# Optimization experiments

Hardware: AMD Instinct MI355X
Metric: run time of the kernel (lower is better)

The kernel has to match this reference:

```python
import jax, jax.numpy as jnp
import numpy as np

T, B, N = 1024, 1024, 64
BETA = 0.9          # bank LIF leak
THRESH = 1.0        # bank threshold
BETA_RO = 0.9       # readout leak
THRESH_RO = 1.0     # readout threshold
CHOSEN_W1 = 0.7
UTE = 1.01


def setup_inputs() -> dict:
    key = jax.random.key(0)
    # sparse binary spike input [T,B,2]
    spike_seq = (jax.random.uniform(key, (T, B, 2)) < 0.05).astype(jnp.float32)
    delays = jnp.arange(1, N + 1, dtype=jnp.int32)
    # per-neuron weights: w1 = chosen_w1, w2 = ute - beta**delay * w1
    w1 = jnp.full((N,), CHOSEN_W1, dtype=jnp.float32)
    w2 = (UTE - (BETA ** delays.astype(jnp.float32)) * CHOSEN_W1).astype(jnp.float32)
    W = jnp.stack([w1, w2], axis=1)  # [N,2]
    return {"spike_seq": spike_seq, "W": W, "delays": delays}


def reference(spike_seq, W, delays):
    Tn, Bn, _ = spike_seq.shape
    Nn = W.shape[0]
    BIG = jnp.iinfo(jnp.int32).max

    def step(carry, xt):
        x_t, t = xt
        bank_mem, ro_mem, inhibit, inhibit_time, winner = carry
        # ---- bank of N LIF neurons (snntorch Leaky, reset='subtract') ----
        cur = x_t @ W.T                                      # [B,N]
        reset = jnp.where(bank_mem > THRESH, THRESH, 0.0)    # reset from prev mem
        bank_mem = BETA * bank_mem + cur - reset
        spk = jnp.where(bank_mem > THRESH, 1.0, 0.0)         # [B,N]
        spk = jnp.where(inhibit, 0.0, spk)                   # global WTA inhibition
        # ---- winner: first step any neuron spikes, pick min-delay spiker ----
        active = jnp.any(spk > 0, axis=0)                    # [N]
        any_active = jnp.any(active)
        cand = jnp.argmin(jnp.where(active, delays, BIG)).astype(jnp.int32)
        winner = jnp.where((winner < 0) & (~inhibit) & any_active, cand, winner)
        # ---- readout LIF (fc_exc = all-ones -> sum over bank) ----
        ro_cur = spk.sum(axis=1, keepdims=True)              # [B,1]
        ro_reset = jnp.where(ro_mem > THRESH_RO, THRESH_RO, 0.0)
        ro_mem = BETA_RO * ro_mem + ro_cur - ro_reset
        ro_spk = jnp.where(ro_mem > THRESH_RO, 1.0, 0.0)     # [B,1]
        fire = jnp.any(ro_spk > 0)
        inhibit_time = jnp.where((~inhibit) & fire, t, inhibit_time)
        inhibit = inhibit | fire
        return (bank_mem, ro_mem, inhibit, inhibit_time, winner), (spk, ro_spk[:, 0])

    init = (jnp.zeros((Bn, Nn), spike_seq.dtype),
            jnp.zeros((Bn, 1), spike_seq.dtype),
            jnp.array(False),
            jnp.int32(-1),
            jnp.int32(-1))
    ts = jnp.arange(Tn, dtype=jnp.int32)
    (_, _, _, inhibit_time, winner), (bank_spk, ro_spk) = jax.lax.scan(step, init, (spike_seq, ts))
    # bank_spk [T,B,N], ro_spk [T,B]; -1 sentinels mean None in the torch code
    return bank_spk, ro_spk, inhibit_time, winner
```

## Files before the change

kernel.cpp:

```cpp
#include <hip/hip_runtime.h>
#include <climits>

#define T_STEPS 1024
#define B_SZ    1024
#define N_NEUR  64
#define BETA    0.9f
#define THRESH  1.0f


__global__ __launch_bounds__(64) void k_init(int* __restrict__ ws) {
  if (threadIdx.x == 0) { ws[0] = INT_MAX; ws[1] = INT_MAX; }
}

__global__ __launch_bounds__(256) void k_phase1(
    const float* __restrict__ x, const float* __restrict__ W,
    int* __restrict__ ws)
{
  const int lane = threadIdx.x & 63;
  const int b = blockIdx.x * 4 + (threadIdx.x >> 6);
  const float w1 = W[lane * 2 + 0];
  const float w2 = W[lane * 2 + 1];
  float mem = 0.0f, ro = 0.0f;
  int tfire = INT_MAX, key = INT_MAX;
  for (int t0 = 0; t0 < T_STEPS; t0 += 64) {
    const float2 xv = *reinterpret_cast<const float2*>(x + ((size_t)(t0 + lane) * B_SZ + b) * 2);
    #pragma unroll
    for (int i = 0; i < 64; ++i) {
      const float x0 = __shfl(xv.x, i);
      const float x1 = __shfl(xv.y, i);
      const float cur = __fadd_rn(__fmul_rn(x0, w1), __fmul_rn(x1, w2));
      const float rst = (mem > THRESH) ? THRESH : 0.0f;
      mem = __fsub_rn(__fadd_rn(__fmul_rn(BETA, mem), cur), rst);
      const unsigned long long msk = __ballot(mem > THRESH);
      if (key == INT_MAX && msk)
        key = ((t0 + i) << 6) | (int)__builtin_ctzll(msk);
      const float rocur = (float)__popcll(msk);
      const float rrst = (ro > THRESH) ? THRESH : 0.0f;
      ro = __fsub_rn(__fadd_rn(__fmul_rn(BETA, ro), rocur), rrst);
      if (tfire == INT_MAX && ro > THRESH) tfire = t0 + i;
    }
    if (tfire != INT_MAX && key != INT_MAX) break;
  }
  if (lane == 0) { atomicMin(&ws[0], tfire); atomicMin(&ws[1], key); }
}

__global__ __launch_bounds__(256) void k_phase2(
    const float* __restrict__ x, const float* __restrict__ W,
    const int* __restrict__ ws, float* __restrict__ out)
{
  const int lane = threadIdx.x & 63;
  const int b = blockIdx.x * 4 + (threadIdx.x >> 6);
  const int Tstar = ws[0];
  const int Tstop = (Tstar < T_STEPS - 1) ? Tstar : (T_STEPS - 1);
  float* __restrict__ outro = out + (size_t)T_STEPS * B_SZ * N_NEUR;
  const float w1 = W[lane * 2 + 0];
  const float w2 = W[lane * 2 + 1];
  float mem = 0.0f, ro = 0.0f;
  for (int t0 = 0; t0 < T_STEPS; t0 += 64) {
    float2 xv = make_float2(0.0f, 0.0f);
    if (t0 <= Tstop)
      xv = *reinterpret_cast<const float2*>(x + ((size_t)(t0 + lane) * B_SZ + b) * 2);
    float myro = 0.0f;
    #pragma unroll 8
    for (int i = 0; i < 64; ++i) {
      const int t = t0 + i;
      float rocur = 0.0f;
      if (t <= Tstop) {
        const float x0 = __shfl(xv.x, i);
        const float x1 = __shfl(xv.y, i);
        const float cur = __fadd_rn(__fmul_rn(x0, w1), __fmul_rn(x1, w2));
        const float rst = (mem > THRESH) ? THRESH : 0.0f;
        mem = __fsub_rn(__fadd_rn(__fmul_rn(BETA, mem), cur), rst);
        const bool s = mem > THRESH;
        out[((size_t)t * B_SZ + b) * N_NEUR + lane] = s ? 1.0f : 0.0f;
        rocur = (float)__popcll(__ballot(s));
      }
      const float rrst = (ro > THRESH) ? THRESH : 0.0f;
      ro = __fsub_rn(__fadd_rn(__fmul_rn(BETA, ro), rocur), rrst);
      const float rospk = (ro > THRESH) ? 1.0f : 0.0f;
      myro = (i == lane) ? rospk : myro;
    }
    outro[(size_t)(t0 + lane) * B_SZ + b] = myro;
  }
  if (blockIdx.x == 0 && threadIdx.x == 0) {
    const int key = ws[1];
    float* sc = outro + (size_t)T_STEPS * B_SZ;
    sc[0] = (Tstar < T_STEPS) ? (float)Tstar : -1.0f;
    sc[1] = (key != INT_MAX) ? (float)(key & 63) : -1.0f;
  }
}

__global__ __launch_bounds__(256) void k_fill(const int* __restrict__ ws, float4* __restrict__ out4) {
  const int Tstar = ws[0];
  const size_t n4 = (size_t)T_STEPS * B_SZ * N_NEUR / 4;
  const size_t stride = (size_t)gridDim.x * blockDim.x;
  for (size_t i = (size_t)blockIdx.x * blockDim.x + threadIdx.x; i < n4; i += stride) {
    const int t = (int)(i >> 14);
    if (t > Tstar) out4[i] = make_float4(0.0f, 0.0f, 0.0f, 0.0f);
  }
}

extern "C" void kernel_launch(void* const* d_in, const int* in_sizes, int n_in,
                              void* d_out, int out_size, void* d_ws, size_t ws_size,
                              hipStream_t stream) {
  const float* x = (const float*)d_in[0];
  const float* W = (const float*)d_in[1];
  float* out = (float*)d_out;
  int* ws = (int*)d_ws;
  k_init  <<<1,        64, 0, stream>>>(ws);
  k_phase1<<<B_SZ / 4, 256, 0, stream>>>(x, W, ws);
  k_phase2<<<B_SZ / 4, 256, 0, stream>>>(x, W, ws, out);
  k_fill  <<<2048,     256, 0, stream>>>(ws, (float4*)out);
}
```

Baseline: 352.2 us.

## Use spike bitmasks, cross-block early exit, and pre-zeroed readout output

Input spikes are turned into per-chunk wave ballot bitmasks, so the current becomes a select of w1/w2 instead of shuffles and multiplies. Phase 1 now publishes its fire time and key through atomicMin after every 64-step chunk and reads back the global minimum, so a wave can stop as soon as another batch has already fired earlier. The fill kernel runs before phase 2 and zeroes the readout region as well, so phase 2 only writes readout ones and can stop once past Tstop. Blocks become single waves, and the init kernel is replaced by a memset. Running the fill before phase 2 adds a write-after-write ordering dependency, and phase 2's early break relies on later readout values staying zero.

```diff
diff --git a/kernel.cpp b/kernel.cpp
--- a/kernel.cpp
+++ b/kernel.cpp
@@ -1,102 +1,109 @@
 #include <hip/hip_runtime.h>
-#include <climits>
 
 #define T_STEPS 1024
 #define B_SZ    1024
 #define N_NEUR  64
-#define BETA    0.9f
-#define THRESH  1.0f
+#define SENT    0x7F7F7F7F
+
+typedef unsigned long long u64;
 
 
-__global__ __launch_bounds__(64) void k_init(int* __restrict__ ws) {
-  if (threadIdx.x == 0) { ws[0] = INT_MAX; ws[1] = INT_MAX; }
-}
-
-__global__ __launch_bounds__(256) void k_phase1(
-    const float* __restrict__ x, const float* __restrict__ W,
-    int* __restrict__ ws)
+__global__ __launch_bounds__(64) void k_phase1(
+    const float* __restrict__ x, const float* __restrict__ W, int* __restrict__ ws)
 {
-  const int lane = threadIdx.x & 63;
-  const int b = blockIdx.x * 4 + (threadIdx.x >> 6);
+  const int lane = threadIdx.x;
+  const int b = blockIdx.x;
   const float w1 = W[lane * 2 + 0];
   const float w2 = W[lane * 2 + 1];
   float mem = 0.0f, ro = 0.0f;
-  int tfire = INT_MAX, key = INT_MAX;
-  for (int t0 = 0; t0 < T_STEPS; t0 += 64) {
-    const float2 xv = *reinterpret_cast<const float2*>(x + ((size_t)(t0 + lane) * B_SZ + b) * 2);
+  int tfire = SENT, key = SENT;
+  for (int c = 0; c < 16; ++c) {
+    const int t0 = c << 6;
+    const float2 v = *reinterpret_cast<const float2*>(x + ((size_t)(t0 + lane) * B_SZ + b) * 2);
+    const u64 m0 = __ballot(v.x != 0.0f);
+    const u64 m1 = __ballot(v.y != 0.0f);
     #pragma unroll
     for (int i = 0; i < 64; ++i) {
-      const float x0 = __shfl(xv.x, i);
-      const float x1 = __shfl(xv.y, i);
-      const float cur = __fadd_rn(__fmul_rn(x0, w1), __fmul_rn(x1, w2));
-      const float rst = (mem > THRESH) ? THRESH : 0.0f;
-      mem = __fsub_rn(__fadd_rn(__fmul_rn(BETA, mem), cur), rst);
-      const unsigned long long msk = __ballot(mem > THRESH);
-      if (key == INT_MAX && msk)
-        key = ((t0 + i) << 6) | (int)__builtin_ctzll(msk);
+      const float cur = __fadd_rn(((m0 >> i) & 1) ? w1 : 0.0f, ((m1 >> i) & 1) ? w2 : 0.0f);
+      const float rst = (mem > 1.0f) ? 1.0f : 0.0f;
+      mem = __fsub_rn(__fadd_rn(__fmul_rn(0.9f, mem), cur), rst);
+      const u64 msk = __ballot(mem > 1.0f);
+      if (key == SENT && msk) key = ((t0 + i) << 6) | (int)__builtin_ctzll(msk);
       const float rocur = (float)__popcll(msk);
-      const float rrst = (ro > THRESH) ? THRESH : 0.0f;
-      ro = __fsub_rn(__fadd_rn(__fmul_rn(BETA, ro), rocur), rrst);
-      if (tfire == INT_MAX && ro > THRESH) tfire = t0 + i;
+      const float rrst = (ro > 1.0f) ? 1.0f : 0.0f;
+      ro = __fsub_rn(__fadd_rn(__fmul_rn(0.9f, ro), rocur), rrst);
+      if (tfire == SENT && ro > 1.0f) tfire = t0 + i;
     }
-    if (tfire != INT_MAX && key != INT_MAX) break;
+    int o0 = SENT, o1 = SENT;
+    if (lane == 0) { o0 = atomicMin(&ws[0], tfire); o1 = atomicMin(&ws[1], key); }
+    o0 = __shfl(o0, 0); o1 = __shfl(o1, 0);
+    const int nt0 = (c + 1) << 6;
+    const bool done_t = (tfire != SENT) || (min(o0, tfire) < nt0);
+    const bool done_k = (key  != SENT) || (min(o1, key)  < (nt0 << 6));
+    if (done_t && done_k) break;
   }
-  if (lane == 0) { atomicMin(&ws[0], tfire); atomicMin(&ws[1], key); }
 }
 
-__global__ __launch_bounds__(256) void k_phase2(
+__global__ __launch_bounds__(256) void k_fill(const int* __restrict__ ws, float* __restrict__ out)
+{
+  const int Tstar = ws[0];
+  float4* out4 = (float4*)out;
+  const size_t n4_bank = (size_t)T_STEPS * B_SZ * N_NEUR / 4;
+  const size_t n4_tot  = n4_bank + (size_t)T_STEPS * B_SZ / 4;
+  const size_t stride = (size_t)gridDim.x * blockDim.x;
+  for (size_t i = (size_t)blockIdx.x * blockDim.x + threadIdx.x; i < n4_tot; i += stride) {
+    if (i >= n4_bank || (int)(i >> 14) > Tstar)
+      out4[i] = make_float4(0.0f, 0.0f, 0.0f, 0.0f);
+  }
+  if (blockIdx.x == 0 && threadIdx.x == 0) {
+    const int key = ws[1];
+    float* sc = out + (size_t)T_STEPS * B_SZ * N_NEUR + (size_t)T_STEPS * B_SZ;
+    sc[0] = (Tstar < T_STEPS) ? (float)Tstar : -1.0f;
+    sc[1] = (key != SENT) ? (float)(key & 63) : -1.0f;
+  }
+}
+
+__global__ __launch_bounds__(64) void k_phase2(
     const float* __restrict__ x, const float* __restrict__ W,
     const int* __restrict__ ws, float* __restrict__ out)
 {
-  const int lane = threadIdx.x & 63;
-  const int b = blockIdx.x * 4 + (threadIdx.x >> 6);
+  const int lane = threadIdx.x;
+  const int b = blockIdx.x;
   const int Tstar = ws[0];
   const int Tstop = (Tstar < T_STEPS - 1) ? Tstar : (T_STEPS - 1);
   float* __restrict__ outro = out + (size_t)T_STEPS * B_SZ * N_NEUR;
   const float w1 = W[lane * 2 + 0];
   const float w2 = W[lane * 2 + 1];
   float mem = 0.0f, ro = 0.0f;
-  for (int t0 = 0; t0 < T_STEPS; t0 += 64) {
-    float2 xv = make_float2(0.0f, 0.0f);
-    if (t0 <= Tstop)
-      xv = *reinterpret_cast<const float2*>(x + ((size_t)(t0 + lane) * B_SZ + b) * 2);
-    float myro = 0.0f;
-    #pragma unroll 8
+  const int lastc = Tstop >> 6;
+  for (int c = 0; c < 16; ++c) {
+    const int t0 = c << 6;
+    u64 m0 = 0, m1 = 0;
+    if (c <= lastc) {
+      const float2 v = *reinterpret_cast<const float2*>(x + ((size_t)(t0 + lane) * B_SZ + b) * 2);
+      m0 = __ballot(v.x != 0.0f);
+      m1 = __ballot(v.y != 0.0f);
+    }
+    u64 romask = 0;
+    #pragma unroll
     for (int i = 0; i < 64; ++i) {
       const int t = t0 + i;
       float rocur = 0.0f;
       if (t <= Tstop) {
-        const float x0 = __shfl(xv.x, i);
-        const float x1 = __shfl(xv.y, i);
-        const float cur = __fadd_rn(__fmul_rn(x0, w1), __fmul_rn(x1, w2));
-        const float rst = (mem > THRESH) ? THRESH : 0.0f;
-        mem = __fsub_rn(__fadd_rn(__fmul_rn(BETA, mem), cur), rst);
-        const bool s = mem > THRESH;
+        const float cur = __fadd_rn(((m0 >> i) & 1) ? w1 : 0.0f, ((m1 >> i) & 1) ? w2 : 0.0f);
+        const float rst = (mem > 1.0f) ? 1.0f : 0.0f;
+        mem = __fsub_rn(__fadd_rn(__fmul_rn(0.9f, mem), cur), rst);
+        const bool s = mem > 1.0f;
         out[((size_t)t * B_SZ + b) * N_NEUR + lane] = s ? 1.0f : 0.0f;
         rocur = (float)__popcll(__ballot(s));
       }
-      const float rrst = (ro > THRESH) ? THRESH : 0.0f;
-      ro = __fsub_rn(__fadd_rn(__fmul_rn(BETA, ro), rocur), rrst);
-      const float rospk = (ro > THRESH) ? 1.0f : 0.0f;
-      myro = (i == lane) ? rospk : myro;
+      const float rrst = (ro > 1.0f) ? 1.0f : 0.0f;
+      ro = __fsub_rn(__fadd_rn(__fmul_rn(0.9f, ro), rocur), rrst);
+      romask |= (u64)(ro > 1.0f) << i;
     }
-    outro[(size_t)(t0 + lane) * B_SZ + b] = myro;
-  }
-  if (blockIdx.x == 0 && threadIdx.x == 0) {
-    const int key = ws[1];
-    float* sc = outro + (size_t)T_STEPS * B_SZ;
-    sc[0] = (Tstar < T_STEPS) ? (float)Tstar : -1.0f;
-    sc[1] = (key != INT_MAX) ? (float)(key & 63) : -1.0f;
-  }
-}
-
-__global__ __launch_bounds__(256) void k_fill(const int* __restrict__ ws, float4* __restrict__ out4) {
-  const int Tstar = ws[0];
-  const size_t n4 = (size_t)T_STEPS * B_SZ * N_NEUR / 4;
-  const size_t stride = (size_t)gridDim.x * blockDim.x;
-  for (size_t i = (size_t)blockIdx.x * blockDim.x + threadIdx.x; i < n4; i += stride) {
-    const int t = (int)(i >> 14);
-    if (t > Tstar) out4[i] = make_float4(0.0f, 0.0f, 0.0f, 0.0f);
+    if ((romask >> lane) & 1)
+      outro[(size_t)(t0 + lane) * B_SZ + b] = 1.0f;
+    if (t0 + 64 > Tstop && !(ro > 1.0f)) break;
   }
 }
 
@@ -107,8 +114,8 @@
   const float* W = (const float*)d_in[1];
   float* out = (float*)d_out;
   int* ws = (int*)d_ws;
-  k_init  <<<1,        64, 0, stream>>>(ws);
-  k_phase1<<<B_SZ / 4, 256, 0, stream>>>(x, W, ws);
-  k_phase2<<<B_SZ / 4, 256, 0, stream>>>(x, W, ws, out);
-  k_fill  <<<2048,     256, 0, stream>>>(ws, (float4*)out);
+  hipMemsetAsync(ws, 0x7F, 8, stream);
+  k_phase1<<<B_SZ, 64, 0, stream>>>(x, W, ws);
+  k_fill  <<<2048, 256, 0, stream>>>(ws, out);
+  k_phase2<<<B_SZ, 64, 0, stream>>>(x, W, ws, out);
 }
```

Measured after the change: 311.4 us. 1.13x faster.
